# Performance work log

Hardware: AMD Instinct MI355X
Metric: run time of the kernel (lower is better)

The kernel has to match this reference:

```python
import jax, jax.numpy as jnp
import numpy as np

D_MODEL = 1024
N_HEADS = 16
HEAD_DIM = D_MODEL // N_HEADS
BATCH = 2
SEQ = 2048


def setup_inputs() -> dict:
    key = jax.random.key(0)
    ks = jax.random.split(key, 7)
    s = 1.0 / np.sqrt(D_MODEL)
    return {
        "x": jax.random.normal(ks[0], (BATCH, SEQ, D_MODEL), dtype=jnp.float32),
        "Wq": jax.random.normal(ks[1], (D_MODEL, D_MODEL), dtype=jnp.float32) * s,
        "Wk": jax.random.normal(ks[2], (D_MODEL, D_MODEL), dtype=jnp.float32) * s,
        "Wv": jax.random.normal(ks[3], (D_MODEL, D_MODEL), dtype=jnp.float32) * s,
        "Wo": jax.random.normal(ks[4], (D_MODEL, D_MODEL), dtype=jnp.float32) * s,
        "Wg": jax.random.normal(ks[5], (D_MODEL, D_MODEL), dtype=jnp.float32) * s,
        "bg": jnp.zeros((D_MODEL,), dtype=jnp.float32),
    }


def _rope_cos_sin(seq_len, head_dim, dtype):
    half = head_dim // 2
    inv_freq = 1.0 / (10000.0 ** (jnp.arange(half, dtype=jnp.float32) / half))
    freqs = jnp.arange(seq_len, dtype=jnp.float32)[:, None] * inv_freq[None, :]  # (S, half)
    emb = jnp.concatenate([freqs, freqs], axis=-1)  # (S, head_dim)
    return jnp.cos(emb).astype(dtype), jnp.sin(emb).astype(dtype)


def _rotate_half(x):
    half = x.shape[-1] // 2
    return jnp.concatenate([-x[..., half:], x[..., :half]], axis=-1)


def reference(x, Wq, Wk, Wv, Wo, Wg, bg):
    bsz, seq_len, d_model = x.shape
    # projections (torch Linear: x @ W.T)
    q = jnp.einsum('bsd,ed->bse', x, Wq).reshape(bsz, seq_len, N_HEADS, HEAD_DIM).transpose(0, 2, 1, 3)
    k = jnp.einsum('bsd,ed->bse', x, Wk).reshape(bsz, seq_len, N_HEADS, HEAD_DIM).transpose(0, 2, 1, 3)
    v = jnp.einsum('bsd,ed->bse', x, Wv).reshape(bsz, seq_len, N_HEADS, HEAD_DIM).transpose(0, 2, 1, 3)
    cos, sin = _rope_cos_sin(seq_len, HEAD_DIM, x.dtype)  # (S, hd)
    cos = cos[None, None]
    sin = sin[None, None]
    q = q * cos + _rotate_half(q) * sin
    k = k * cos + _rotate_half(k) * sin
    scores = jnp.einsum('bhqd,bhkd->bhqk', q, k) / jnp.sqrt(jnp.asarray(HEAD_DIM, x.dtype))
    causal = jnp.triu(jnp.full((seq_len, seq_len), -jnp.inf, dtype=x.dtype), k=1)
    scores = scores + causal
    probs = jax.nn.softmax(scores, axis=-1)
    attn = jnp.einsum('bhqk,bhkd->bhqd', probs, v)  # (B,H,S,hd)
    attn = attn.transpose(0, 2, 1, 3).reshape(bsz, seq_len, d_model)
    out = jnp.einsum('bsd,ed->bse', attn, Wo)
    gate = jax.nn.sigmoid(jnp.einsum('bsd,ed->bse', out, Wg) + bg)
    return out * gate
```

## Files before the change

kernel.cpp:

```cpp
#include <hip/hip_runtime.h>

#define DM 1024
#define NH 16
#define HD 64
#define BATCH 2
#define SEQ 2048
#define MROWS (BATCH*SEQ)

typedef unsigned short u16;
typedef unsigned long long u64;
typedef __bf16 bf16x8 __attribute__((ext_vector_type(8)));
typedef float f32x4 __attribute__((ext_vector_type(4)));
typedef unsigned int u32x4 __attribute__((ext_vector_type(4)));
typedef unsigned int __attribute__((address_space(1))) as1_uint;
typedef unsigned int __attribute__((address_space(3))) as3_uint;

__device__ __forceinline__ u16 f2bf(float f) {
  unsigned u = __builtin_bit_cast(unsigned, f);
  u += 0x7fffu + ((u >> 16) & 1u);
  return (u16)(u >> 16);
}
__device__ __forceinline__ float bf2f(u16 h) {
  return __builtin_bit_cast(float, ((unsigned)h) << 16);
}
__device__ __forceinline__ bf16x8 ld8(const u16* p) {
  return __builtin_bit_cast(bf16x8, *reinterpret_cast<const u32x4*>(p));
}
__device__ __forceinline__ void gl_lds16(const u16* g, void* lds) {
  __builtin_amdgcn_global_load_lds((const as1_uint*)(const void*)g,
                                   (as3_uint*)lds, 16, 0, 0);
}
__device__ __forceinline__ unsigned pk2(float a, float b) {
  return __builtin_amdgcn_perm(__builtin_bit_cast(unsigned, a),
                               __builtin_bit_cast(unsigned, b), 0x07060302u);
}

__global__ void conv_kernel(const float* __restrict__ in, u16* __restrict__ out, int n) {
  int i = (blockIdx.x * 256 + threadIdx.x) * 4;
  if (i >= n) return;
  f32x4 v = *reinterpret_cast<const f32x4*>(in + i);
  out[i + 0] = f2bf(v[0]);
  out[i + 1] = f2bf(v[1]);
  out[i + 2] = f2bf(v[2]);
  out[i + 3] = f2bf(v[3]);
}

__global__ void tab_kernel(float* __restrict__ tab) {
  int t = blockIdx.x * 256 + threadIdx.x;
  if (t >= SEQ * 32) return;
  int s = t >> 5, i = t & 31;
  float inv = powf(10000.0f, -(float)i / 32.0f);
  float f = (float)s * inv;
  tab[s * 64 + i] = cosf(f);
  tab[s * 64 + 32 + i] = sinf(f);
}

template <int MODE>
__global__ __launch_bounds__(256) void gemm_bt(
    const u16* __restrict__ A, const u16* __restrict__ B,
    u16* __restrict__ Cbf, float* __restrict__ Cf,
    const float* __restrict__ bias, const float* __restrict__ mult,
    int M, int N, int K, size_t bz, size_t cz) {
  B += blockIdx.z * bz;
  u16* Cb = Cbf + blockIdx.z * cz;
  const int m0 = blockIdx.y * 128, n0 = blockIdx.x * 64;
  const int t = threadIdx.x, w = t >> 6;
  const int l = t & 63;
  const int wr = w >> 1, wc = w & 1;
  const int lr = l & 15, lg = l >> 4;
  __shared__ __align__(16) u16 As[128 * 32];
  __shared__ __align__(16) u16 Bs[64 * 32];
  f32x4 acc[4][2] = {};
  const int srow = t >> 2;
  const int sc8 = (t & 3) * 8;
  const u16* gA = A + (size_t)(m0 + srow) * K + sc8;
  const u16* gB = B + (size_t)(n0 + srow) * K + sc8;
  char* lA = (char*)As + w * 1024;
  char* lB = (char*)Bs + w * 1024;
  const size_t rstep = (size_t)64 * K;

  for (int kt = 0; kt < K; kt += 32) {
    gl_lds16(gA + kt, lA);
    gl_lds16(gA + kt + rstep, lA + 4096);
    gl_lds16(gB + kt, lB);
    __syncthreads();
    bf16x8 af[4], bfr[2];
#pragma unroll
    for (int i = 0; i < 4; ++i)
      af[i] = ld8(&As[(wr * 64 + i * 16 + lr) * 32 + lg * 8]);
#pragma unroll
    for (int i = 0; i < 2; ++i)
      bfr[i] = ld8(&Bs[(wc * 32 + i * 16 + lr) * 32 + lg * 8]);
#pragma unroll
    for (int mi = 0; mi < 4; ++mi)
#pragma unroll
      for (int ni = 0; ni < 2; ++ni)
        acc[mi][ni] = __builtin_amdgcn_mfma_f32_16x16x32_bf16(af[mi], bfr[ni], acc[mi][ni], 0, 0, 0);
    __syncthreads();
  }
#pragma unroll
  for (int mi = 0; mi < 4; ++mi)
#pragma unroll
    for (int ni = 0; ni < 2; ++ni)
#pragma unroll
      for (int r = 0; r < 4; ++r) {
        int row = m0 + wr * 64 + mi * 16 + lg * 4 + r;
        int col = n0 + wc * 32 + ni * 16 + lr;
        size_t idx = (size_t)row * N + col;
        float v = acc[mi][ni][r];
        if constexpr (MODE == 0) {
          Cb[idx] = f2bf(v);
        } else if constexpr (MODE == 1) {
          Cf[idx] = v;
          Cb[idx] = f2bf(v);
        } else {
          float g = 1.0f / (1.0f + __expf(-(v + bias[col])));
          Cf[idx] = mult[idx] * g;
        }
      }
}

__global__ void rope_kernel(const u16* __restrict__ Qin, const u16* __restrict__ Kin,
                            u16* __restrict__ Qr, u16* __restrict__ Kr,
                            const float* __restrict__ tab) {
  int t = blockIdx.x * 256 + threadIdx.x;
  int i = t & 31;
  int s = (t >> 5) & (SEQ - 1);
  int bh = t >> 16;
  if (bh >= BATCH * NH) return;
  int b = bh >> 4, h = bh & 15;
  size_t ib = ((size_t)(b * SEQ + s)) * DM + h * 64;
  size_t ob = ((size_t)bh * SEQ + s) * 64;
  float c = tab[s * 64 + i], sn = tab[s * 64 + 32 + i];
  float q1 = bf2f(Qin[ib + i]), q2 = bf2f(Qin[ib + 32 + i]);
  float k1 = bf2f(Kin[ib + i]), k2 = bf2f(Kin[ib + 32 + i]);
  Qr[ob + i] = f2bf(q1 * c - q2 * sn);
  Qr[ob + 32 + i] = f2bf(q2 * c + q1 * sn);
  Kr[ob + i] = f2bf(k1 * c - k2 * sn);
  Kr[ob + 32 + i] = f2bf(k2 * c + k1 * sn);
}

__global__ __launch_bounds__(256) void vtrans_kernel(const u16* __restrict__ Vin,
                                                     u16* __restrict__ Vt) {
  const int s0 = blockIdx.x * 64;
  const int bh = blockIdx.y;
  const int b = bh >> 4, h = bh & 15;
  const int t = threadIdx.x;
  __shared__ __align__(16) u16 T[64][72];
  const int row = t >> 3, col = (t & 7) * 8;
#pragma unroll
  for (int p = 0; p < 2; ++p) {
    int r = p * 32 + row;
    *reinterpret_cast<u32x4*>(&T[r][col]) =
        *reinterpret_cast<const u32x4*>(&Vin[(size_t)(b * SEQ + s0 + r) * DM + h * 64 + col]);
  }
  __syncthreads();
  const size_t ob = (size_t)bh * 64 * SEQ;
#pragma unroll
  for (int p = 0; p < 2; ++p) {
    int dr = p * 32 + row;
    u16 tmp[8];
#pragma unroll
    for (int j = 0; j < 8; ++j) tmp[j] = T[col + j][dr];
    *reinterpret_cast<u32x4*>(&Vt[ob + (size_t)dr * SEQ + s0 + col]) =
        *reinterpret_cast<u32x4*>(tmp);
  }
}

__global__ __launch_bounds__(256) void attn_kernel(
    const u16* __restrict__ Q, const u16* __restrict__ K, const u16* __restrict__ Vt,
    u16* __restrict__ O) {
  const int bh = blockIdx.y;
  int qb = blockIdx.x;
  if (bh & 1) qb = (gridDim.x - 1) - qb;
  const int t = threadIdx.x, w = t >> 6, l = t & 63;
  const int lr = l & 15, lg = l >> 4;
  const int qw0 = qb * 128 + w * 32;
  const size_t base = (size_t)bh * SEQ * 64;
  const size_t vbase = (size_t)bh * 64 * SEQ;
  __shared__ __align__(16) u16 Ks[2][64 * 64];
  __shared__ __align__(16) u16 Vs[2][64 * 64];
  __shared__ __align__(16) u16 Ps[4][2][1024];

  bf16x8 qf[2][2];
#pragma unroll
  for (int qs = 0; qs < 2; ++qs) {
    const u16* qp = &Q[base + (size_t)(qw0 + qs * 16 + lr) * 64 + lg * 8];
    qf[qs][0] = ld8(qp);
    qf[qs][1] = ld8(qp + 32);
  }

  f32x4 oacc[2][4] = {};
  float l_run[2] = {0.0f, 0.0f};

  const int nt = (qb + 1) * 2;
  const int srow = t >> 3, sc16 = t & 7;
  const int lo0 = srow * 128 + ((sc16 * 16) ^ ((srow & 7) << 4));
  const int lo1 = lo0 + 4096;
  const u16* Kg = K + base + sc16 * 8;
  const u16* Vg = Vt + vbase + sc16 * 8;
  u32x4 rg[4];

#define LOADG(tile) do { const int kv_ = (tile) * 64;                     \
    rg[0] = *(const u32x4*)(Kg + (size_t)(kv_ + srow) * 64);              \
    rg[1] = *(const u32x4*)(Kg + (size_t)(kv_ + srow + 32) * 64);         \
    rg[2] = *(const u32x4*)(Vg + (size_t)srow * SEQ + kv_);               \
    rg[3] = *(const u32x4*)(Vg + (size_t)(srow + 32) * SEQ + kv_); } while (0)

#define WRITEL(tile) do { char* kb_ = (char*)Ks[(tile) & 1];              \
    char* vb_ = (char*)Vs[(tile) & 1];                                    \
    *(u32x4*)(kb_ + lo0) = rg[0]; *(u32x4*)(kb_ + lo1) = rg[1];           \
    *(u32x4*)(vb_ + lo0) = rg[2]; *(u32x4*)(vb_ + lo1) = rg[3]; } while (0)

  LOADG(0);
  WRITEL(0);
  __syncthreads();

  for (int tk = 0; tk < nt; ++tk) {
    const int cur = tk & 1;
    const int kv0 = tk * 64;
    if (tk + 1 < nt) LOADG(tk + 1);
    const char* kb = (const char*)Ks[cur];
    const char* vb = (const char*)Vs[cur];
    if (kv0 <= qw0 + 31) {
      bf16x8 kf[4][2];
      const int swk = (lr & 7) << 4;
#pragma unroll
      for (int h = 0; h < 4; ++h) {
        const char* rp = kb + (h * 16 + lr) * 128;
        kf[h][0] = *(const bf16x8*)(rp + ((lg * 16) ^ swk));
        kf[h][1] = *(const bf16x8*)(rp + ((64 + lg * 16) ^ swk));
      }
      const int qslo = (kv0 <= qw0 + 15) ? 0 : 1;
      const int swz = (lr & 7) << 4;
#pragma unroll
      for (int qs = 0; qs < 2; ++qs) {
        if (qs < qslo) continue;
        const int qs0 = qw0 + qs * 16;
        f32x4 st[4];
#pragma unroll
        for (int h = 0; h < 4; ++h) {
          f32x4 z = {};
          z = __builtin_amdgcn_mfma_f32_16x16x32_bf16(kf[h][0], qf[qs][0], z, 0, 0, 0);
          z = __builtin_amdgcn_mfma_f32_16x16x32_bf16(kf[h][1], qf[qs][1], z, 0, 0, 0);
          st[h] = z;
        }
        float pv[4][4];
#pragma unroll
        for (int h = 0; h < 4; ++h)
#pragma unroll
          for (int r = 0; r < 4; ++r)
            pv[h][r] = fmaf(st[h][r], 0.1803368801f, -12.0f);
        if (kv0 + 63 > qs0) {
#pragma unroll
          for (int h = 0; h < 4; ++h)
#pragma unroll
            for (int r = 0; r < 4; ++r)
              if (kv0 + h * 16 + lg * 4 + r > qs0 + lr) pv[h][r] = -1e30f;
        }
        float hs[4];
#pragma unroll
        for (int h = 0; h < 4; ++h) {
#pragma unroll
          for (int r = 0; r < 4; ++r) pv[h][r] = exp2f(pv[h][r]);
          hs[h] = (pv[h][0] + pv[h][1]) + (pv[h][2] + pv[h][3]);
        }
        float ts = (hs[0] + hs[1]) + (hs[2] + hs[3]);
        ts += __shfl_xor(ts, 16);
        ts += __shfl_xor(ts, 32);
        l_run[qs] += ts;
        char* pq = (char*)Ps[w][qs];
#pragma unroll
        for (int h = 0; h < 4; ++h) {
          u64 pw = (u64)pk2(pv[h][1], pv[h][0]) | ((u64)pk2(pv[h][3], pv[h][2]) << 32);
          *(u64*)(pq + ((((h >> 1) * 512 + lr * 32 + (h & 1) * 16 + lg * 4) * 2) ^ swz)) = pw;
        }
      }
#pragma unroll
      for (int ks = 0; ks < 2; ++ks) {
        bf16x8 pf[2];
#pragma unroll
        for (int qs = 0; qs < 2; ++qs)
          if (qs >= qslo)
            pf[qs] = *(const bf16x8*)((char*)Ps[w][qs] +
                                      ((ks * 1024 + lr * 64 + lg * 16) ^ swz));
#pragma unroll
        for (int dc = 0; dc < 4; ++dc) {
          const int row = dc * 16 + lr;
          bf16x8 vf = *(const bf16x8*)(vb + row * 128 +
                                       (((ks * 64) + lg * 16) ^ ((lr & 7) << 4)));
#pragma unroll
          for (int qs = 0; qs < 2; ++qs)
            if (qs >= qslo)
              oacc[qs][dc] = __builtin_amdgcn_mfma_f32_16x16x32_bf16(pf[qs], vf, oacc[qs][dc], 0, 0, 0);
        }
      }
    }
    if (tk + 1 < nt) {
      WRITEL(tk + 1);
      __syncthreads();
    }
  }
#undef LOADG
#undef WRITEL
  const int b = bh >> 4, hh = bh & 15;
#pragma unroll
  for (int qs = 0; qs < 2; ++qs) {
    const int qs0 = qw0 + qs * 16;
#pragma unroll
    for (int r = 0; r < 4; ++r) {
      float inv = 1.0f / __shfl(l_run[qs], lg * 4 + r);
#pragma unroll
      for (int dc = 0; dc < 4; ++dc)
        O[((size_t)(b * SEQ + qs0 + lg * 4 + r)) * DM + hh * 64 + dc * 16 + lr] =
            f2bf(oacc[qs][dc][r] * inv);
    }
  }
}

extern "C" void kernel_launch(void* const* d_in, const int* in_sizes, int n_in,
                              void* d_out, int out_size, void* d_ws, size_t ws_size,
                              hipStream_t stream) {
  const float* x = (const float*)d_in[0];
  const float* Wq = (const float*)d_in[1];
  const float* Wk = (const float*)d_in[2];
  const float* Wv = (const float*)d_in[3];
  const float* Wo = (const float*)d_in[4];
  const float* Wg = (const float*)d_in[5];
  const float* bg = (const float*)d_in[6];
  float* out = (float*)d_out;

  const size_t NX = (size_t)MROWS * DM;
  const size_t NW = (size_t)DM * DM;
  u16* xbf = (u16*)d_ws;
  u16* wbf = xbf + NX;
  u16* qkv = wbf + 5 * NW;
  u16* qkvr = qkv + 3 * NX;
  u16* attn = qkvr + 3 * NX;
  u16* outbf = attn + NX;
  float* outf = (float*)(outbf + NX);
  float* tab = outf + NX;

  conv_kernel<<<NX / 1024, 256, 0, stream>>>(x, xbf, (int)NX);
  conv_kernel<<<NW / 1024, 256, 0, stream>>>(Wq, wbf + 0 * NW, (int)NW);
  conv_kernel<<<NW / 1024, 256, 0, stream>>>(Wk, wbf + 1 * NW, (int)NW);
  conv_kernel<<<NW / 1024, 256, 0, stream>>>(Wv, wbf + 2 * NW, (int)NW);
  conv_kernel<<<NW / 1024, 256, 0, stream>>>(Wo, wbf + 3 * NW, (int)NW);
  conv_kernel<<<NW / 1024, 256, 0, stream>>>(Wg, wbf + 4 * NW, (int)NW);
  tab_kernel<<<(SEQ * 32) / 256, 256, 0, stream>>>(tab);
  gemm_bt<0><<<dim3(DM / 64, MROWS / 128, 3), 256, 0, stream>>>(
      xbf, wbf, qkv, nullptr, nullptr, nullptr, MROWS, DM, DM, NW, NX);
  rope_kernel<<<(BATCH * NH * SEQ * 32) / 256, 256, 0, stream>>>(
      qkv, qkv + NX, qkvr, qkvr + NX, tab);
  vtrans_kernel<<<dim3(SEQ / 64, BATCH * NH), 256, 0, stream>>>(
      qkv + 2 * NX, qkvr + 2 * NX);
  attn_kernel<<<dim3(SEQ / 128, BATCH * NH), 256, 0, stream>>>(
      qkvr, qkvr + NX, qkvr + 2 * NX, attn);
  gemm_bt<1><<<dim3(DM / 64, MROWS / 128, 1), 256, 0, stream>>>(
      attn, wbf + 3 * NW, outbf, outf, nullptr, nullptr, MROWS, DM, DM, 0, 0);
  gemm_bt<2><<<dim3(DM / 64, MROWS / 128, 1), 256, 0, stream>>>(
      outbf, wbf + 4 * NW, nullptr, out, bg, outf, MROWS, DM, DM, 0, 0);
}
```

Baseline: 281.8 us.

## Fuse conversion kernels and remap GEMM and attention blocks for XCD cache locality

Merges the six fp32-to-bf16 conversion launches into one kernel that picks its source by index range, which removes launch overhead. The GEMM block index is remapped so each group of consecutive hardware-dispatched blocks (interleaved across 8 XCDs) shares nearby tiles. The attention grid is remapped so each XCD handles a fixed set of heads, which should improve L2 reuse of K/V. The swizzles assume the block counts divide evenly by 8 and that the attention grid is exactly 16x32.

```diff
diff --git a/kernel.cpp b/kernel.cpp
--- a/kernel.cpp
+++ b/kernel.cpp
@@ -35,10 +35,22 @@
                                __builtin_bit_cast(unsigned, b), 0x07060302u);
 }
 
-__global__ void conv_kernel(const float* __restrict__ in, u16* __restrict__ out, int n) {
-  int i = (blockIdx.x * 256 + threadIdx.x) * 4;
-  if (i >= n) return;
-  f32x4 v = *reinterpret_cast<const f32x4*>(in + i);
+__global__ void convall_kernel(const float* __restrict__ x,
+                               const float* __restrict__ w0, const float* __restrict__ w1,
+                               const float* __restrict__ w2, const float* __restrict__ w3,
+                               const float* __restrict__ w4, u16* __restrict__ out) {
+  const size_t NX = (size_t)MROWS * DM;
+  size_t i = ((size_t)blockIdx.x * 256 + threadIdx.x) * 4;
+  const float* src;
+  size_t off;
+  if (i < NX) { src = x; off = i; }
+  else {
+    size_t j = i - NX;
+    int wsel = (int)(j >> 20);
+    off = j & ((1u << 20) - 1);
+    src = (wsel == 0) ? w0 : (wsel == 1) ? w1 : (wsel == 2) ? w2 : (wsel == 3) ? w3 : w4;
+  }
+  f32x4 v = *reinterpret_cast<const f32x4*>(src + off);
   out[i + 0] = f2bf(v[0]);
   out[i + 1] = f2bf(v[1]);
   out[i + 2] = f2bf(v[2]);
@@ -63,7 +75,18 @@
     int M, int N, int K, size_t bz, size_t cz) {
   B += blockIdx.z * bz;
   u16* Cb = Cbf + blockIdx.z * cz;
-  const int m0 = blockIdx.y * 128, n0 = blockIdx.x * 64;
+  const int gx = gridDim.x;
+  {
+    int nwg = gx * gridDim.y;
+    int flat = blockIdx.y * gx + blockIdx.x;
+    flat = (flat & 7) * (nwg >> 3) + (flat >> 3);
+    const int bx = flat % gx, by = flat / gx;
+    A += (size_t)by * 128 * K;
+    B += (size_t)bx * 64 * K;
+    Cb += (size_t)by * 128 * N + bx * 64;
+    if constexpr (MODE != 0) Cf += (size_t)by * 128 * N + bx * 64;
+    if constexpr (MODE == 2) { bias += bx * 64; mult += (size_t)by * 128 * N + bx * 64; }
+  }
   const int t = threadIdx.x, w = t >> 6;
   const int l = t & 63;
   const int wr = w >> 1, wc = w & 1;
@@ -73,8 +96,8 @@
   f32x4 acc[4][2] = {};
   const int srow = t >> 2;
   const int sc8 = (t & 3) * 8;
-  const u16* gA = A + (size_t)(m0 + srow) * K + sc8;
-  const u16* gB = B + (size_t)(n0 + srow) * K + sc8;
+  const u16* gA = A + (size_t)srow * K + sc8;
+  const u16* gB = B + (size_t)srow * K + sc8;
   char* lA = (char*)As + w * 1024;
   char* lB = (char*)Bs + w * 1024;
   const size_t rstep = (size_t)64 * K;
@@ -104,8 +127,8 @@
     for (int ni = 0; ni < 2; ++ni)
 #pragma unroll
       for (int r = 0; r < 4; ++r) {
-        int row = m0 + wr * 64 + mi * 16 + lg * 4 + r;
-        int col = n0 + wc * 32 + ni * 16 + lr;
+        int row = wr * 64 + mi * 16 + lg * 4 + r;
+        int col = wc * 32 + ni * 16 + lr;
         size_t idx = (size_t)row * N + col;
         float v = acc[mi][ni][r];
         if constexpr (MODE == 0) {
@@ -170,9 +193,14 @@
 __global__ __launch_bounds__(256) void attn_kernel(
     const u16* __restrict__ Q, const u16* __restrict__ K, const u16* __restrict__ Vt,
     u16* __restrict__ O) {
-  const int bh = blockIdx.y;
-  int qb = blockIdx.x;
-  if (bh & 1) qb = (gridDim.x - 1) - qb;
+  const int qb_raw = blockIdx.x;
+  const int bh_raw = blockIdx.y;
+  const int xs = qb_raw & 7, hi = qb_raw >> 3;
+  const int lo = bh_raw & 15, rr = bh_raw >> 4;
+  const int bh = xs * 4 + (lo & 3);
+  const int q0i = hi + 2 * (lo >> 2);
+  const int qb = rr ? (15 - q0i) : q0i;
+
   const int t = threadIdx.x, w = t >> 6, l = t & 63;
   const int lr = l & 15, lg = l >> 4;
   const int qw0 = qb * 128 + w * 32;
@@ -341,12 +369,7 @@
   float* outf = (float*)(outbf + NX);
   float* tab = outf + NX;
 
-  conv_kernel<<<NX / 1024, 256, 0, stream>>>(x, xbf, (int)NX);
-  conv_kernel<<<NW / 1024, 256, 0, stream>>>(Wq, wbf + 0 * NW, (int)NW);
-  conv_kernel<<<NW / 1024, 256, 0, stream>>>(Wk, wbf + 1 * NW, (int)NW);
-  conv_kernel<<<NW / 1024, 256, 0, stream>>>(Wv, wbf + 2 * NW, (int)NW);
-  conv_kernel<<<NW / 1024, 256, 0, stream>>>(Wo, wbf + 3 * NW, (int)NW);
-  conv_kernel<<<NW / 1024, 256, 0, stream>>>(Wg, wbf + 4 * NW, (int)NW);
+  convall_kernel<<<(NX + 5 * NW) / 1024, 256, 0, stream>>>(x, Wq, Wk, Wv, Wo, Wg, xbf);
   tab_kernel<<<(SEQ * 32) / 256, 256, 0, stream>>>(tab);
   gemm_bt<0><<<dim3(DM / 64, MROWS / 128, 3), 256, 0, stream>>>(
       xbf, wbf, qkv, nullptr, nullptr, nullptr, MROWS, DM, DM, NW, NX);
```

New measurement: 251.7 us. -10.7%, faster.
